# Kernel optimization log

Measured on AMD Instinct MI355X. Metric: run time of the kernel, lower is better.

## Reference

```python
import jax, jax.numpy as jnp
import numpy as np

EMBED_DIM = 1024
NUM_HEADS = 16
HEAD_DIM = EMBED_DIM // NUM_HEADS
B, L = 2, 2048
SCALE = HEAD_DIM ** -0.5


def setup_inputs() -> dict:
    key = jax.random.key(0)
    ks = jax.random.split(key, 8)
    x = jax.random.normal(ks[0], (B, L, EMBED_DIM), dtype=jnp.float32)
    phylo_dists = jax.random.uniform(ks[1], (B, L), dtype=jnp.float32)
    alibi_bias = jax.random.normal(ks[2], (NUM_HEADS, L, L), dtype=jnp.float32) * 0.02
    # causal mask: 1 where attending allowed (j <= i), broadcast over B,H
    attn_mask = (jnp.arange(L)[:, None] >= jnp.arange(L)[None, :])[None, None]
    # learned params (Linear stores weight as [out, in]; y = x @ W.T + b)
    qkv_w = jax.random.normal(ks[3], (3 * EMBED_DIM, EMBED_DIM), dtype=jnp.float32) * (EMBED_DIM ** -0.5)
    qkv_b = jnp.zeros((3 * EMBED_DIM,), dtype=jnp.float32)
    out_w = jax.random.normal(ks[4], (EMBED_DIM, EMBED_DIM), dtype=jnp.float32) * (EMBED_DIM ** -0.5)
    out_b = jnp.zeros((EMBED_DIM,), dtype=jnp.float32)
    phylo_alpha = jnp.float32(0.5)
    return {"x": x, "phylo_dists": phylo_dists, "alibi_bias": alibi_bias,
            "attn_mask": attn_mask, "qkv_w": qkv_w, "qkv_b": qkv_b,
            "out_w": out_w, "out_b": out_b, "phylo_alpha": phylo_alpha}


def reference(x, phylo_dists, alibi_bias, attn_mask, qkv_w, qkv_b, out_w, out_b, phylo_alpha):
    Bm, Lm, D = x.shape
    qkv = (x @ qkv_w.T + qkv_b).reshape(Bm, Lm, 3, NUM_HEADS, HEAD_DIM)
    qkv = jnp.transpose(qkv, (2, 0, 3, 1, 4))  # [3, B, H, L, hd]
    q, k, v = qkv[0], qkv[1], qkv[2]
    # phylo temperature: scalar per batch element
    phylo_scalar = phylo_dists.mean(axis=-1).reshape(Bm, 1, 1, 1)
    temp = jnp.clip(1.0 + phylo_alpha * phylo_scalar, 1e-6, None)
    scores = jnp.einsum('bhqd,bhkd->bhqk', q, k) * (SCALE * temp)
    scores = scores + alibi_bias[None]  # [B,H,L,L]
    scores = jnp.where(attn_mask, scores, -jnp.inf)
    attn = jax.nn.softmax(scores, axis=-1)
    out = jnp.einsum('bhqk,bhkd->bhqd', attn, v)
    out = jnp.transpose(out, (0, 2, 1, 3)).reshape(Bm, Lm, D)
    return out @ out_w.T + out_b
```

## Files before the change

kernel.cpp:

```cpp
#include <hip/hip_runtime.h>
#include <hip/hip_bf16.h>

typedef __attribute__((ext_vector_type(8))) short bf16x8;
typedef __attribute__((ext_vector_type(4))) float f32x4;
typedef __attribute__((ext_vector_type(4))) float f4v;
typedef __attribute__((ext_vector_type(4))) short s4v;

__device__ __forceinline__ short f2bf(float f) {
    union { __hip_bfloat16 h; short s; } u;
    u.h = __float2bfloat16(f);
    return u.s;
}

__device__ __forceinline__ void gload_lds16(const void* g, void* l) {
    __builtin_amdgcn_global_load_lds(
        (const __attribute__((address_space(1))) void*)g,
        (__attribute__((address_space(3))) void*)l,
        16, 0, 0);
}

#define MFMA16(a, b, c) __builtin_amdgcn_mfma_f32_16x16x32_bf16((a), (b), (c), 0, 0, 0)

__global__ void prep_kernel(const float* __restrict__ x,
                            const float* __restrict__ qw,
                            const float* __restrict__ ow,
                            const float* __restrict__ pd,
                            const float* __restrict__ alphap,
                            s4v* __restrict__ xb, s4v* __restrict__ qb,
                            s4v* __restrict__ ob, float* __restrict__ scales) {
    __shared__ float wsum[4];
    if (blockIdx.x >= 2048) {
        int b = blockIdx.x - 2048;
        float s = 0.f;
        for (int i = threadIdx.x; i < 2048; i += 256) s += pd[b * 2048 + i];
        for (int o = 32; o; o >>= 1) s += __shfl_down(s, o);
        if ((threadIdx.x & 63) == 0) wsum[threadIdx.x >> 6] = s;
        __syncthreads();
        if (threadIdx.x == 0) {
            float t = wsum[0] + wsum[1] + wsum[2] + wsum[3];
            float mean = t * (1.0f / 2048.0f);
            float temp = fmaxf(1.0f + alphap[0] * mean, 1e-6f);
            scales[b] = 0.125f * temp;
        }
        return;
    }
    #pragma unroll
    for (int j = 0; j < 4; ++j) {
        int idx = blockIdx.x * 1024 + j * 256 + threadIdx.x;
        const f4v* src;
        s4v* dst;
        int off;
        if (idx < 1048576)      { src = (const f4v*)x;  dst = xb; off = idx; }
        else if (idx < 1835008) { src = (const f4v*)qw; dst = qb; off = idx - 1048576; }
        else                    { src = (const f4v*)ow; dst = ob; off = idx - 1835008; }
        f4v v = src[off];
        s4v o;
        #pragma unroll
        for (int k = 0; k < 4; ++k) o[k] = f2bf(v[k]);
        dst[off] = o;
    }
}

template<int BF16_OUT, int NF>
__global__ __launch_bounds__(256, 2)
void gemm_nt(const __hip_bfloat16* __restrict__ A,
             const __hip_bfloat16* __restrict__ Bw,
             const float* __restrict__ bias,
             void* __restrict__ Cv,
             int M, int N, int K) {
    __shared__ short sA[128 * 64];
    __shared__ short sB[NF * 32 * 64];
    const int tid = threadIdx.x;
    const int wave = tid >> 6, lane = tid & 63;
    const int g = lane >> 4, c = lane & 15;
    const int wr = wave >> 1, wc = wave & 1;
    const long m0 = (long)blockIdx.y * 128, n0 = (long)blockIdx.x * (NF * 32);

    f32x4 acc[4][NF];
    #pragma unroll
    for (int m = 0; m < 4; ++m)
        #pragma unroll
        for (int n = 0; n < NF; ++n) acc[m][n] = f32x4{0.f, 0.f, 0.f, 0.f};

    for (int k0 = 0; k0 < K; k0 += 64) {
        #pragma unroll
        for (int i = 0; i < 4; ++i) {
            int cb = (i * 4 + wave) * 64;
            int chunk = cb + lane;
            int row = chunk >> 3;
            int sc = ((chunk & 7) * 16) ^ ((row & 7) << 4);
            const char* gA = (const char*)(A + (m0 + row) * (long)K + k0) + sc;
            gload_lds16(gA, (char*)sA + cb * 16);
        }
        #pragma unroll
        for (int i = 0; i < NF; ++i) {
            int cb = (i * 4 + wave) * 64;
            int chunk = cb + lane;
            int row = chunk >> 3;
            int sc = ((chunk & 7) * 16) ^ ((row & 7) << 4);
            const char* gB = (const char*)(Bw + (n0 + row) * (long)K + k0) + sc;
            gload_lds16(gB, (char*)sB + cb * 16);
        }
        __syncthreads();
        #pragma unroll
        for (int s = 0; s < 2; ++s) {
            bf16x8 af[4], bfr[NF];
            #pragma unroll
            for (int m = 0; m < 4; ++m) {
                int row = wr * 64 + m * 16 + c;
                int kb = (s * 64 + g * 16) ^ ((row & 7) << 4);
                af[m] = *(const bf16x8*)((const char*)sA + row * 128 + kb);
            }
            #pragma unroll
            for (int n = 0; n < NF; ++n) {
                int row = wc * (NF * 16) + n * 16 + c;
                int kb = (s * 64 + g * 16) ^ ((row & 7) << 4);
                bfr[n] = *(const bf16x8*)((const char*)sB + row * 128 + kb);
            }
            #pragma unroll
            for (int m = 0; m < 4; ++m)
                #pragma unroll
                for (int n = 0; n < NF; ++n)
                    acc[m][n] = MFMA16(af[m], bfr[n], acc[m][n]);
        }
        __syncthreads();
    }

    #pragma unroll
    for (int m = 0; m < 4; ++m) {
        #pragma unroll
        for (int n = 0; n < NF; ++n) {
            long col = n0 + wc * (NF * 16) + n * 16 + c;
            float bv = bias[col];
            #pragma unroll
            for (int r = 0; r < 4; ++r) {
                long row = m0 + wr * 64 + m * 16 + g * 4 + r;
                float v = acc[m][n][r] + bv;
                if (BF16_OUT)
                    ((__hip_bfloat16*)Cv)[row * N + col] = __float2bfloat16(v);
                else
                    ((float*)Cv)[row * N + col] = v;
            }
        }
    }
}


__device__ __forceinline__ void compute_tile(
    const short* sKc, const short* sVtc, short* sPw,
    bf16x8 qf0, bf16x8 qf1,
    f32x4 (&acc_o)[4], f32x4& accL, float (&m)[4],
    const float (&ab)[4][4],
    float scale, int qi0, int kv0, bool diag, int g, int c)
{
    f32x4 accs[4];
    const int swz = (c & 7) << 4;
    __builtin_amdgcn_s_setprio(1);
    #pragma unroll
    for (int nf = 0; nf < 4; ++nf) {
        const char* kb = (const char*)sKc + (nf * 16 + c) * 128;
        bf16x8 kf0 = *(const bf16x8*)(kb + ((g * 16) ^ swz));
        bf16x8 kf1 = *(const bf16x8*)(kb + ((64 + g * 16) ^ swz));
        accs[nf] = f32x4{0.f, 0.f, 0.f, 0.f};
        accs[nf] = MFMA16(qf0, kf0, accs[nf]);
        accs[nf] = MFMA16(qf1, kf1, accs[nf]);
    }
    __builtin_amdgcn_s_setprio(0);
    float s[4][4], pmax[4];
    bool ok = true;
    #pragma unroll
    for (int r = 0; r < 4; ++r) {
        int qi = qi0 + r;
        #pragma unroll
        for (int nf = 0; nf < 4; ++nf) {
            float sv = fmaf(accs[nf][r], scale, ab[nf][r]);
            if (diag && (kv0 + nf * 16 + c > qi)) sv = -1e30f;
            s[r][nf] = sv;
        }
        pmax[r] = fmaxf(fmaxf(s[r][0], s[r][1]), fmaxf(s[r][2], s[r][3]));
        ok = ok && (pmax[r] <= m[r] + 8.0f);
    }
    if (!__all(ok)) {
        #pragma unroll
        for (int r = 0; r < 4; ++r) {
            float mx = pmax[r];
            mx = fmaxf(mx, __shfl_xor(mx, 1));
            mx = fmaxf(mx, __shfl_xor(mx, 2));
            mx = fmaxf(mx, __shfl_xor(mx, 4));
            mx = fmaxf(mx, __shfl_xor(mx, 8));
            float mn = fmaxf(m[r], mx);
            float alpha = __expf(m[r] - mn);
            m[r] = mn;
            accL[r] *= alpha;
            #pragma unroll
            for (int d = 0; d < 4; ++d) acc_o[d][r] *= alpha;
        }
    }
    #pragma unroll
    for (int r = 0; r < 4; ++r)
        #pragma unroll
        for (int nf = 0; nf < 4; ++nf)
            sPw[(g * 4 + r) * 72 + nf * 16 + c] = f2bf(__expf(s[r][nf] - m[r]));
    asm volatile("s_waitcnt lgkmcnt(0)" ::: "memory");
    bf16x8 pf0 = *(const bf16x8*)((const char*)sPw + c * 144 + g * 16);
    bf16x8 pf1 = *(const bf16x8*)((const char*)sPw + c * 144 + 64 + g * 16);
    const short ONE = 0x3F80;
    const bf16x8 ones = {ONE, ONE, ONE, ONE, ONE, ONE, ONE, ONE};
    __builtin_amdgcn_s_setprio(1);
    accL = MFMA16(pf0, ones, accL);
    accL = MFMA16(pf1, ones, accL);
    #pragma unroll
    for (int d = 0; d < 4; ++d) {
        const char* vb = (const char*)sVtc + (d * 16 + c) * 144;
        bf16x8 vf0 = *(const bf16x8*)(vb + g * 16);
        bf16x8 vf1 = *(const bf16x8*)(vb + 64 + g * 16);
        acc_o[d] = MFMA16(pf0, vf0, acc_o[d]);
        acc_o[d] = MFMA16(pf1, vf1, acc_o[d]);
    }
    __builtin_amdgcn_s_setprio(0);
}

__global__ __launch_bounds__(256, 3)
void attn_kernel(const __hip_bfloat16* __restrict__ qkv,
                 const float* __restrict__ alibi,
                 const float* __restrict__ scales,
                 __hip_bfloat16* __restrict__ out) {
    __shared__ short sK[2][64 * 64];
    __shared__ short sVt[2][64 * 72];
    __shared__ short sP[4][16 * 72];

    const int h = blockIdx.x, b = blockIdx.y;
    const int qt = 31 - blockIdx.z;
    const int nIter = qt + 1;
    const int tid = threadIdx.x;
    const int wave = tid >> 6, lane = tid & 63;
    const int g = lane >> 4, c = lane & 15;
    const float scale = scales[b];
    const long base_bl = (long)b * 2048;

    const int q0 = qt * 64 + wave * 16;

    const __hip_bfloat16* qrow = qkv + (base_bl + q0 + c) * 3072 + h * 64;
    bf16x8 qf0 = *(const bf16x8*)(qrow + g * 8);
    bf16x8 qf1 = *(const bf16x8*)(qrow + 32 + g * 8);

    const __hip_bfloat16* kg = qkv + base_bl * 3072 + 1024 + h * 64;
    const __hip_bfloat16* vg = qkv + base_bl * 3072 + 2048 + h * 64;
    const float* ab_base = alibi + (long)h * 2048 * 2048 + (long)(q0 + g * 4) * 2048;

    const int p2 = tid & 31;
    const int d0 = (tid >> 5) * 8;
    const __hip_bfloat16* vrow = vg + (long)(2 * p2) * 3072 + d0;

    f32x4 acc[4], accL;
    float m[4];
    #pragma unroll
    for (int d = 0; d < 4; ++d) acc[d] = f32x4{0.f, 0.f, 0.f, 0.f};
    accL = f32x4{0.f, 0.f, 0.f, 0.f};
    #pragma unroll
    for (int r = 0; r < 4; ++r) m[r] = -3e38f;

    float ab[4][4], abn[4][4];

    {
        #pragma unroll
        for (int i = 0; i < 2; ++i) {
            int cb = (i * 4 + wave) * 64;
            int chunk = cb + lane;
            int row = chunk >> 3;
            int sc = ((chunk & 7) * 16) ^ ((row & 7) << 4);
            gload_lds16((const char*)(kg + (long)row * 3072) + sc,
                        (char*)sK[0] + cb * 16);
        }
        bf16x8 va = *(const bf16x8*)vrow;
        bf16x8 vb = *(const bf16x8*)(vrow + 3072);
        #pragma unroll
        for (int j = 0; j < 8; ++j) {
            unsigned pk = ((unsigned)(unsigned short)va[j]) |
                          (((unsigned)(unsigned short)vb[j]) << 16);
            *(unsigned*)((char*)sVt[0] + (d0 + j) * 144 + p2 * 4) = pk;
        }
        #pragma unroll
        for (int nf = 0; nf < 4; ++nf)
            #pragma unroll
            for (int r = 0; r < 4; ++r) {
                ab[nf][r] = ab_base[(long)r * 2048 + nf * 16 + c];
                abn[nf][r] = 0.f;
            }
    }
    __syncthreads();

    for (int t = 0; t < nIter; ++t) {
        const int cur = t & 1;
        const int kv0 = t * 64;
        bf16x8 va, vb;
        const bool haveNext = (t + 1 < nIter);
        if (haveNext) {
            #pragma unroll
            for (int i = 0; i < 2; ++i) {
                int cb = (i * 4 + wave) * 64;
                int chunk = cb + lane;
                int row = chunk >> 3;
                int sc = ((chunk & 7) * 16) ^ ((row & 7) << 4);
                gload_lds16((const char*)(kg + (long)(kv0 + 64 + row) * 3072) + sc,
                            (char*)sK[cur ^ 1] + cb * 16);
            }
            const __hip_bfloat16* vp = vrow + (long)(kv0 + 64) * 3072;
            va = *(const bf16x8*)vp;
            vb = *(const bf16x8*)(vp + 3072);
            #pragma unroll
            for (int nf = 0; nf < 4; ++nf)
                #pragma unroll
                for (int r = 0; r < 4; ++r)
                    abn[nf][r] = ab_base[(long)r * 2048 + kv0 + 64 + nf * 16 + c];
        }

        compute_tile(sK[cur], sVt[cur], &sP[wave][0], qf0, qf1,
                     acc, accL, m, ab, scale, q0 + g * 4, kv0, t == qt, g, c);

        if (haveNext) {
            #pragma unroll
            for (int j = 0; j < 8; ++j) {
                unsigned pk = ((unsigned)(unsigned short)va[j]) |
                              (((unsigned)(unsigned short)vb[j]) << 16);
                *(unsigned*)((char*)sVt[cur ^ 1] + (d0 + j) * 144 + p2 * 4) = pk;
            }
        }
        __syncthreads();
        #pragma unroll
        for (int nf = 0; nf < 4; ++nf)
            #pragma unroll
            for (int r = 0; r < 4; ++r)
                ab[nf][r] = abn[nf][r];
    }

    __hip_bfloat16* op = out + (base_bl + q0 + g * 4) * 1024 + h * 64;
    #pragma unroll
    for (int r = 0; r < 4; ++r) {
        float inv = 1.0f / accL[r];
        #pragma unroll
        for (int d = 0; d < 4; ++d)
            op[(long)r * 1024 + d * 16 + c] = __float2bfloat16(acc[d][r] * inv);
    }
}

extern "C" void kernel_launch(void* const* d_in, const int* in_sizes, int n_in,
                              void* d_out, int out_size, void* d_ws, size_t ws_size,
                              hipStream_t stream) {
    const float* x      = (const float*)d_in[0];
    const float* phylo  = (const float*)d_in[1];
    const float* alibi  = (const float*)d_in[2];
    const float* qkv_w  = (const float*)d_in[4];
    const float* qkv_b  = (const float*)d_in[5];
    const float* out_w  = (const float*)d_in[6];
    const float* out_b  = (const float*)d_in[7];
    const float* alphap = (const float*)d_in[8];

    char* ws = (char*)d_ws;
    __hip_bfloat16* xbf   = (__hip_bfloat16*)(ws);
    __hip_bfloat16* qwbf  = (__hip_bfloat16*)(ws + (8l << 20));
    __hip_bfloat16* owbf  = (__hip_bfloat16*)(ws + (14l << 20));
    __hip_bfloat16* qkvbf = (__hip_bfloat16*)(ws + (16l << 20));
    __hip_bfloat16* aobf  = (__hip_bfloat16*)(ws + (40l << 20));
    float* scales         = (float*)(ws + (48l << 20));

    prep_kernel<<<2050, 256, 0, stream>>>(x, qkv_w, out_w, phylo, alphap,
                                          (s4v*)xbf, (s4v*)qwbf, (s4v*)owbf, scales);

    gemm_nt<1, 4><<<dim3(24, 32), 256, 0, stream>>>(xbf, qwbf, qkv_b, qkvbf,
                                                    4096, 3072, 1024);
    attn_kernel<<<dim3(16, 2, 32), 256, 0, stream>>>(qkvbf, alibi, scales, aobf);
    gemm_nt<0, 2><<<dim3(16, 32), 256, 0, stream>>>(aobf, owbf, out_b, d_out,
                                                    4096, 1024, 1024);
}
```

Baseline: 127.8 us.

## Compute transposed scores so P stays in registers, dropping LDS round-trip

Swaps the MFMA operands so each lane holds one query's scores across key positions. The exponentiated probabilities can then be fed directly as the B operand of 16x16x16 MFMAs for the PV product, with no write and read through per-wave shared memory. Row sums are now taken with register adds and two shuffles instead of extra MFMAs against a ones vector, and the V stride is changed to 74. In exchange the PV product uses twice as many smaller-K MFMAs, and the alibi loads and output stores change access patterns.

Result: slower. 214.0 us (+67.4%).

```diff
diff --git a/kernel.cpp b/kernel.cpp
--- a/kernel.cpp
+++ b/kernel.cpp
@@ -2,6 +2,7 @@
 #include <hip/hip_bf16.h>
 
 typedef __attribute__((ext_vector_type(8))) short bf16x8;
+typedef __attribute__((ext_vector_type(4))) short bf16x4;
 typedef __attribute__((ext_vector_type(4))) float f32x4;
 typedef __attribute__((ext_vector_type(4))) float f4v;
 typedef __attribute__((ext_vector_type(4))) short s4v;
@@ -20,6 +21,7 @@
 }
 
 #define MFMA16(a, b, c) __builtin_amdgcn_mfma_f32_16x16x32_bf16((a), (b), (c), 0, 0, 0)
+#define MFMA16K16(a, b, c) __builtin_amdgcn_mfma_f32_16x16x16bf16_1k((a), (b), (c), 0, 0, 0)
 
 __global__ void prep_kernel(const float* __restrict__ x,
                             const float* __restrict__ qw,
@@ -146,79 +148,7 @@
 }
 
 
-__device__ __forceinline__ void compute_tile(
-    const short* sKc, const short* sVtc, short* sPw,
-    bf16x8 qf0, bf16x8 qf1,
-    f32x4 (&acc_o)[4], f32x4& accL, float (&m)[4],
-    const float (&ab)[4][4],
-    float scale, int qi0, int kv0, bool diag, int g, int c)
-{
-    f32x4 accs[4];
-    const int swz = (c & 7) << 4;
-    __builtin_amdgcn_s_setprio(1);
-    #pragma unroll
-    for (int nf = 0; nf < 4; ++nf) {
-        const char* kb = (const char*)sKc + (nf * 16 + c) * 128;
-        bf16x8 kf0 = *(const bf16x8*)(kb + ((g * 16) ^ swz));
-        bf16x8 kf1 = *(const bf16x8*)(kb + ((64 + g * 16) ^ swz));
-        accs[nf] = f32x4{0.f, 0.f, 0.f, 0.f};
-        accs[nf] = MFMA16(qf0, kf0, accs[nf]);
-        accs[nf] = MFMA16(qf1, kf1, accs[nf]);
-    }
-    __builtin_amdgcn_s_setprio(0);
-    float s[4][4], pmax[4];
-    bool ok = true;
-    #pragma unroll
-    for (int r = 0; r < 4; ++r) {
-        int qi = qi0 + r;
-        #pragma unroll
-        for (int nf = 0; nf < 4; ++nf) {
-            float sv = fmaf(accs[nf][r], scale, ab[nf][r]);
-            if (diag && (kv0 + nf * 16 + c > qi)) sv = -1e30f;
-            s[r][nf] = sv;
-        }
-        pmax[r] = fmaxf(fmaxf(s[r][0], s[r][1]), fmaxf(s[r][2], s[r][3]));
-        ok = ok && (pmax[r] <= m[r] + 8.0f);
-    }
-    if (!__all(ok)) {
-        #pragma unroll
-        for (int r = 0; r < 4; ++r) {
-            float mx = pmax[r];
-            mx = fmaxf(mx, __shfl_xor(mx, 1));
-            mx = fmaxf(mx, __shfl_xor(mx, 2));
-            mx = fmaxf(mx, __shfl_xor(mx, 4));
-            mx = fmaxf(mx, __shfl_xor(mx, 8));
-            float mn = fmaxf(m[r], mx);
-            float alpha = __expf(m[r] - mn);
-            m[r] = mn;
-            accL[r] *= alpha;
-            #pragma unroll
-            for (int d = 0; d < 4; ++d) acc_o[d][r] *= alpha;
-        }
-    }
-    #pragma unroll
-    for (int r = 0; r < 4; ++r)
-        #pragma unroll
-        for (int nf = 0; nf < 4; ++nf)
-            sPw[(g * 4 + r) * 72 + nf * 16 + c] = f2bf(__expf(s[r][nf] - m[r]));
-    asm volatile("s_waitcnt lgkmcnt(0)" ::: "memory");
-    bf16x8 pf0 = *(const bf16x8*)((const char*)sPw + c * 144 + g * 16);
-    bf16x8 pf1 = *(const bf16x8*)((const char*)sPw + c * 144 + 64 + g * 16);
-    const short ONE = 0x3F80;
-    const bf16x8 ones = {ONE, ONE, ONE, ONE, ONE, ONE, ONE, ONE};
-    __builtin_amdgcn_s_setprio(1);
-    accL = MFMA16(pf0, ones, accL);
-    accL = MFMA16(pf1, ones, accL);
-    #pragma unroll
-    for (int d = 0; d < 4; ++d) {
-        const char* vb = (const char*)sVtc + (d * 16 + c) * 144;
-        bf16x8 vf0 = *(const bf16x8*)(vb + g * 16);
-        bf16x8 vf1 = *(const bf16x8*)(vb + 64 + g * 16);
-        acc_o[d] = MFMA16(pf0, vf0, acc_o[d]);
-        acc_o[d] = MFMA16(pf1, vf1, acc_o[d]);
-    }
-    __builtin_amdgcn_s_setprio(0);
-}
+#define VSTRIDE 74
 
 __global__ __launch_bounds__(256, 3)
 void attn_kernel(const __hip_bfloat16* __restrict__ qkv,
@@ -226,8 +156,7 @@
                  const float* __restrict__ scales,
                  __hip_bfloat16* __restrict__ out) {
     __shared__ short sK[2][64 * 64];
-    __shared__ short sVt[2][64 * 72];
-    __shared__ short sP[4][16 * 72];
+    __shared__ short sVt[2][64 * VSTRIDE];
 
     const int h = blockIdx.x, b = blockIdx.y;
     const int qt = 31 - blockIdx.z;
@@ -238,27 +167,25 @@
     const float scale = scales[b];
     const long base_bl = (long)b * 2048;
 
-    const int q0 = qt * 64 + wave * 16;
-
-    const __hip_bfloat16* qrow = qkv + (base_bl + q0 + c) * 3072 + h * 64;
+    const int q0w = qt * 64 + wave * 16;
+    const int q_lane = q0w + c;
+
+    const __hip_bfloat16* qrow = qkv + (base_bl + q_lane) * 3072 + h * 64;
     bf16x8 qf0 = *(const bf16x8*)(qrow + g * 8);
     bf16x8 qf1 = *(const bf16x8*)(qrow + 32 + g * 8);
 
     const __hip_bfloat16* kg = qkv + base_bl * 3072 + 1024 + h * 64;
     const __hip_bfloat16* vg = qkv + base_bl * 3072 + 2048 + h * 64;
-    const float* ab_base = alibi + (long)h * 2048 * 2048 + (long)(q0 + g * 4) * 2048;
+    const float* ab_base = alibi + (long)h * 2048 * 2048 + (long)q_lane * 2048 + g * 4;
 
     const int p2 = tid & 31;
     const int d0 = (tid >> 5) * 8;
     const __hip_bfloat16* vrow = vg + (long)(2 * p2) * 3072 + d0;
 
-    f32x4 acc[4], accL;
-    float m[4];
+    f32x4 acc[4];
+    float accL = 0.f, m = -3e38f;
     #pragma unroll
     for (int d = 0; d < 4; ++d) acc[d] = f32x4{0.f, 0.f, 0.f, 0.f};
-    accL = f32x4{0.f, 0.f, 0.f, 0.f};
-    #pragma unroll
-    for (int r = 0; r < 4; ++r) m[r] = -3e38f;
 
     float ab[4][4], abn[4][4];
 
@@ -278,13 +205,13 @@
         for (int j = 0; j < 8; ++j) {
             unsigned pk = ((unsigned)(unsigned short)va[j]) |
                           (((unsigned)(unsigned short)vb[j]) << 16);
-            *(unsigned*)((char*)sVt[0] + (d0 + j) * 144 + p2 * 4) = pk;
+            *(unsigned*)((char*)sVt[0] + (d0 + j) * (VSTRIDE * 2) + p2 * 4) = pk;
         }
         #pragma unroll
         for (int nf = 0; nf < 4; ++nf)
             #pragma unroll
             for (int r = 0; r < 4; ++r) {
-                ab[nf][r] = ab_base[(long)r * 2048 + nf * 16 + c];
+                ab[nf][r] = ab_base[nf * 16 + r];
                 abn[nf][r] = 0.f;
             }
     }
@@ -312,18 +239,91 @@
             for (int nf = 0; nf < 4; ++nf)
                 #pragma unroll
                 for (int r = 0; r < 4; ++r)
-                    abn[nf][r] = ab_base[(long)r * 2048 + kv0 + 64 + nf * 16 + c];
-        }
-
-        compute_tile(sK[cur], sVt[cur], &sP[wave][0], qf0, qf1,
-                     acc, accL, m, ab, scale, q0 + g * 4, kv0, t == qt, g, c);
+                    abn[nf][r] = ab_base[kv0 + 64 + nf * 16 + r];
+        }
+
+        {
+            const short* sKc = sK[cur];
+            const short* sVtc = sVt[cur];
+            const bool diag = (t == qt);
+            f32x4 accs[4];
+            const int swz = (c & 7) << 4;
+            __builtin_amdgcn_s_setprio(1);
+            #pragma unroll
+            for (int nf = 0; nf < 4; ++nf) {
+                const char* kb = (const char*)sKc + (nf * 16 + c) * 128;
+                bf16x8 kf0 = *(const bf16x8*)(kb + ((g * 16) ^ swz));
+                bf16x8 kf1 = *(const bf16x8*)(kb + ((64 + g * 16) ^ swz));
+                accs[nf] = f32x4{0.f, 0.f, 0.f, 0.f};
+                accs[nf] = MFMA16(kf0, qf0, accs[nf]);
+                accs[nf] = MFMA16(kf1, qf1, accs[nf]);
+            }
+            __builtin_amdgcn_s_setprio(0);
+
+            float s[4][4];
+            float pmax = -3e38f;
+            #pragma unroll
+            for (int nf = 0; nf < 4; ++nf)
+                #pragma unroll
+                for (int r = 0; r < 4; ++r) {
+                    float sv = fmaf(accs[nf][r], scale, ab[nf][r]);
+                    if (diag && (kv0 + nf * 16 + g * 4 + r > q_lane)) sv = -1e30f;
+                    s[nf][r] = sv;
+                    pmax = fmaxf(pmax, sv);
+                }
+            bool ok = (pmax <= m + 8.0f);
+            if (!__all(ok)) {
+                float mx = fmaxf(pmax, __shfl_xor(pmax, 16));
+                mx = fmaxf(mx, __shfl_xor(mx, 32));
+                float mn = fmaxf(m, mx);
+                float alpha = __expf(m - mn);
+                m = mn;
+                accL *= alpha;
+                #pragma unroll
+                for (int d = 0; d < 4; ++d)
+                    #pragma unroll
+                    for (int r = 0; r < 4; ++r) acc[d][r] *= alpha;
+            }
+            unsigned pw[4][2];
+            float ls = 0.f;
+            #pragma unroll
+            for (int nf = 0; nf < 4; ++nf) {
+                float e0 = __expf(s[nf][0] - m);
+                float e1 = __expf(s[nf][1] - m);
+                float e2 = __expf(s[nf][2] - m);
+                float e3 = __expf(s[nf][3] - m);
+                ls += (e0 + e1) + (e2 + e3);
+                pw[nf][0] = ((unsigned)(unsigned short)f2bf(e0)) |
+                            (((unsigned)(unsigned short)f2bf(e1)) << 16);
+                pw[nf][1] = ((unsigned)(unsigned short)f2bf(e2)) |
+                            (((unsigned)(unsigned short)f2bf(e3)) << 16);
+            }
+            ls += __shfl_xor(ls, 16);
+            ls += __shfl_xor(ls, 32);
+            accL += ls;
+
+            __builtin_amdgcn_s_setprio(1);
+            #pragma unroll
+            for (int df = 0; df < 4; ++df) {
+                const char* vb2 = (const char*)sVtc + (df * 16 + c) * (VSTRIDE * 2);
+                #pragma unroll
+                for (int nf = 0; nf < 4; ++nf) {
+                    bf16x4 vf = *(const bf16x4*)(vb2 + (nf * 16 + g * 4) * 2);
+                    union { unsigned w[2]; bf16x4 v; } pu;
+                    pu.w[0] = pw[nf][0];
+                    pu.w[1] = pw[nf][1];
+                    acc[df] = MFMA16K16(vf, pu.v, acc[df]);
+                }
+            }
+            __builtin_amdgcn_s_setprio(0);
+        }
 
         if (haveNext) {
             #pragma unroll
             for (int j = 0; j < 8; ++j) {
                 unsigned pk = ((unsigned)(unsigned short)va[j]) |
                               (((unsigned)(unsigned short)vb[j]) << 16);
-                *(unsigned*)((char*)sVt[cur ^ 1] + (d0 + j) * 144 + p2 * 4) = pk;
+                *(unsigned*)((char*)sVt[cur ^ 1] + (d0 + j) * (VSTRIDE * 2) + p2 * 4) = pk;
             }
         }
         __syncthreads();
@@ -334,13 +334,14 @@
                 ab[nf][r] = abn[nf][r];
     }
 
-    __hip_bfloat16* op = out + (base_bl + q0 + g * 4) * 1024 + h * 64;
-    #pragma unroll
-    for (int r = 0; r < 4; ++r) {
-        float inv = 1.0f / accL[r];
-        #pragma unroll
-        for (int d = 0; d < 4; ++d)
-            op[(long)r * 1024 + d * 16 + c] = __float2bfloat16(acc[d][r] * inv);
+    __hip_bfloat16* op = out + (base_bl + q_lane) * 1024 + h * 64;
+    float inv = 1.0f / accL;
+    #pragma unroll
+    for (int df = 0; df < 4; ++df) {
+        s4v o;
+        #pragma unroll
+        for (int r = 0; r < 4; ++r) o[r] = f2bf(acc[df][r] * inv);
+        *(s4v*)(op + df * 16 + g * 4) = o;
     }
 }
 
```

## Split KV range for long causal query tiles and merge partials

Applied to the files above, without the earlier changes.

The upper 16 query tiles of the causal attention now run as two blocks, each covering half of the KV range, instead of one long block. Partial outputs and their (max, sum) statistics go to workspace, and a new merge kernel combines them with log-sum-exp weights. The aim is to shorten the longest blocks and balance work across CUs. The cost is an extra kernel launch, extra global traffic for the partials, and bf16 rounding of the partials before the merge.

Measured after the change: 136.8 us. 1.07x slower.

```diff
diff --git a/kernel.cpp b/kernel.cpp
--- a/kernel.cpp
+++ b/kernel.cpp
@@ -10,6 +10,12 @@
     union { __hip_bfloat16 h; short s; } u;
     u.h = __float2bfloat16(f);
     return u.s;
+}
+
+__device__ __forceinline__ float bf2f(short s) {
+    union { short s; __hip_bfloat16 h; } u;
+    u.s = s;
+    return __bfloat162float(u.h);
 }
 
 __device__ __forceinline__ void gload_lds16(const void* g, void* l) {
@@ -224,14 +230,29 @@
 void attn_kernel(const __hip_bfloat16* __restrict__ qkv,
                  const float* __restrict__ alibi,
                  const float* __restrict__ scales,
-                 __hip_bfloat16* __restrict__ out) {
+                 __hip_bfloat16* __restrict__ out,
+                 __hip_bfloat16* __restrict__ pO,
+                 float2* __restrict__ pML) {
     __shared__ short sK[2][64 * 64];
     __shared__ short sVt[2][64 * 72];
     __shared__ short sP[4][16 * 72];
 
     const int h = blockIdx.x, b = blockIdx.y;
-    const int qt = 31 - blockIdx.z;
-    const int nIter = qt + 1;
+    const int z = blockIdx.z;
+    int qt, t0, t1, split;
+    if (z < 32) {
+        qt = 31 - (z >> 1);
+        split = z & 1;
+        int nIter = qt + 1;
+        int half = nIter >> 1;
+        t0 = split ? half : 0;
+        t1 = split ? nIter : half;
+    } else {
+        qt = 47 - z;
+        split = -1;
+        t0 = 0;
+        t1 = qt + 1;
+    }
     const int tid = threadIdx.x;
     const int wave = tid >> 6, lane = tid & 63;
     const int g = lane >> 4, c = lane & 15;
@@ -263,38 +284,40 @@
     float ab[4][4], abn[4][4];
 
     {
+        const int kvp = t0 * 64;
         #pragma unroll
         for (int i = 0; i < 2; ++i) {
             int cb = (i * 4 + wave) * 64;
             int chunk = cb + lane;
             int row = chunk >> 3;
             int sc = ((chunk & 7) * 16) ^ ((row & 7) << 4);
-            gload_lds16((const char*)(kg + (long)row * 3072) + sc,
-                        (char*)sK[0] + cb * 16);
-        }
-        bf16x8 va = *(const bf16x8*)vrow;
-        bf16x8 vb = *(const bf16x8*)(vrow + 3072);
+            gload_lds16((const char*)(kg + (long)(kvp + row) * 3072) + sc,
+                        (char*)sK[t0 & 1] + cb * 16);
+        }
+        const __hip_bfloat16* vp = vrow + (long)kvp * 3072;
+        bf16x8 va = *(const bf16x8*)vp;
+        bf16x8 vb = *(const bf16x8*)(vp + 3072);
         #pragma unroll
         for (int j = 0; j < 8; ++j) {
             unsigned pk = ((unsigned)(unsigned short)va[j]) |
                           (((unsigned)(unsigned short)vb[j]) << 16);
-            *(unsigned*)((char*)sVt[0] + (d0 + j) * 144 + p2 * 4) = pk;
+            *(unsigned*)((char*)sVt[t0 & 1] + (d0 + j) * 144 + p2 * 4) = pk;
         }
         #pragma unroll
         for (int nf = 0; nf < 4; ++nf)
             #pragma unroll
             for (int r = 0; r < 4; ++r) {
-                ab[nf][r] = ab_base[(long)r * 2048 + nf * 16 + c];
+                ab[nf][r] = ab_base[(long)r * 2048 + kvp + nf * 16 + c];
                 abn[nf][r] = 0.f;
             }
     }
     __syncthreads();
 
-    for (int t = 0; t < nIter; ++t) {
+    for (int t = t0; t < t1; ++t) {
         const int cur = t & 1;
         const int kv0 = t * 64;
         bf16x8 va, vb;
-        const bool haveNext = (t + 1 < nIter);
+        const bool haveNext = (t + 1 < t1);
         if (haveNext) {
             #pragma unroll
             for (int i = 0; i < 2; ++i) {
@@ -334,13 +357,58 @@
                 ab[nf][r] = abn[nf][r];
     }
 
-    __hip_bfloat16* op = out + (base_bl + q0 + g * 4) * 1024 + h * 64;
-    #pragma unroll
-    for (int r = 0; r < 4; ++r) {
-        float inv = 1.0f / accL[r];
-        #pragma unroll
-        for (int d = 0; d < 4; ++d)
-            op[(long)r * 1024 + d * 16 + c] = __float2bfloat16(acc[d][r] * inv);
+    if (split >= 0) {
+        const long pbase = ((((long)b * 16 + h) * 16 + (qt - 16)) * 2 + split) * 64;
+        #pragma unroll
+        for (int r = 0; r < 4; ++r) {
+            int ql = wave * 16 + g * 4 + r;
+            float invL = 1.0f / accL[r];
+            __hip_bfloat16* pp = pO + (pbase + ql) * 64;
+            #pragma unroll
+            for (int d = 0; d < 4; ++d)
+                pp[d * 16 + c] = __float2bfloat16(acc[d][r] * invL);
+            if (c == 0) pML[pbase + ql] = float2{m[r], accL[r]};
+        }
+    } else {
+        __hip_bfloat16* op = out + (base_bl + q0 + g * 4) * 1024 + h * 64;
+        #pragma unroll
+        for (int r = 0; r < 4; ++r) {
+            float inv = 1.0f / accL[r];
+            #pragma unroll
+            for (int d = 0; d < 4; ++d)
+                op[(long)r * 1024 + d * 16 + c] = __float2bfloat16(acc[d][r] * inv);
+        }
+    }
+}
+
+__global__ void merge_kernel(const __hip_bfloat16* __restrict__ pO,
+                             const float2* __restrict__ pML,
+                             __hip_bfloat16* __restrict__ out) {
+    const int qt = 16 + blockIdx.x;
+    const int h = blockIdx.y, b = blockIdx.z;
+    const int t = threadIdx.x;
+    const int row = t >> 2;
+    const int c0 = (t & 3) << 4;
+    const long base = (((long)b * 16 + h) * 16 + blockIdx.x) * 2;
+    float2 ml1 = pML[(base + 0) * 64 + row];
+    float2 ml2 = pML[(base + 1) * 64 + row];
+    float M = fmaxf(ml1.x, ml2.x);
+    float w1 = __expf(ml1.x - M) * ml1.y;
+    float w2 = __expf(ml2.x - M) * ml2.y;
+    float inv = 1.0f / (w1 + w2);
+    w1 *= inv;
+    w2 *= inv;
+    const bf16x8* p1 = (const bf16x8*)(pO + ((base + 0) * 64 + row) * 64 + c0);
+    const bf16x8* p2 = (const bf16x8*)(pO + ((base + 1) * 64 + row) * 64 + c0);
+    __hip_bfloat16* op = out + ((long)b * 2048 + (long)qt * 64 + row) * 1024 + h * 64 + c0;
+    #pragma unroll
+    for (int k = 0; k < 2; ++k) {
+        bf16x8 a = p1[k], bv = p2[k];
+        bf16x8 o;
+        #pragma unroll
+        for (int j = 0; j < 8; ++j)
+            o[j] = f2bf(bf2f(a[j]) * w1 + bf2f(bv[j]) * w2);
+        *(bf16x8*)(op + k * 8) = o;
     }
 }
 
@@ -363,13 +431,17 @@
     __hip_bfloat16* qkvbf = (__hip_bfloat16*)(ws + (16l << 20));
     __hip_bfloat16* aobf  = (__hip_bfloat16*)(ws + (40l << 20));
     float* scales         = (float*)(ws + (48l << 20));
+    __hip_bfloat16* pO    = (__hip_bfloat16*)(ws);
+    float2* pML           = (float2*)(ws + (8l << 20));
 
     prep_kernel<<<2050, 256, 0, stream>>>(x, qkv_w, out_w, phylo, alphap,
                                           (s4v*)xbf, (s4v*)qwbf, (s4v*)owbf, scales);
 
     gemm_nt<1, 4><<<dim3(24, 32), 256, 0, stream>>>(xbf, qwbf, qkv_b, qkvbf,
                                                     4096, 3072, 1024);
-    attn_kernel<<<dim3(16, 2, 32), 256, 0, stream>>>(qkvbf, alibi, scales, aobf);
+    attn_kernel<<<dim3(16, 2, 48), 256, 0, stream>>>(qkvbf, alibi, scales, aobf,
+                                                     pO, pML);
+    merge_kernel<<<dim3(16, 16, 2), 256, 0, stream>>>(pO, pML, aobf);
     gemm_nt<0, 2><<<dim3(16, 32), 256, 0, stream>>>(aobf, owbf, out_b, d_out,
                                                     4096, 1024, 1024);
 }
```

## Pair complementary causal query tiles in one 512-thread attention block

Applied to the files above, without the earlier changes.

Each attention block now has 8 waves and handles two query tiles, p and 31-p, so every block walks the same number of KV tiles and the causal work is balanced across blocks. The K/V tiles staged in LDS are shared by both query tiles, which halves K/V global loads per query. Waves on the shorter tile skip compute once past their diagonal but still hit the barriers. The grid halves to 512 blocks, which lowers parallelism and raises register and LDS pressure per block.

Result: no change. 129.8 us (+1.5%).

```diff
diff --git a/kernel.cpp b/kernel.cpp
--- a/kernel.cpp
+++ b/kernel.cpp
@@ -220,25 +220,26 @@
     __builtin_amdgcn_s_setprio(0);
 }
 
-__global__ __launch_bounds__(256, 3)
+__global__ __launch_bounds__(512, 4)
 void attn_kernel(const __hip_bfloat16* __restrict__ qkv,
                  const float* __restrict__ alibi,
                  const float* __restrict__ scales,
                  __hip_bfloat16* __restrict__ out) {
     __shared__ short sK[2][64 * 64];
     __shared__ short sVt[2][64 * 72];
-    __shared__ short sP[4][16 * 72];
+    __shared__ short sP[8][16 * 72];
 
     const int h = blockIdx.x, b = blockIdx.y;
-    const int qt = 31 - blockIdx.z;
-    const int nIter = qt + 1;
+    const int p = blockIdx.z;
     const int tid = threadIdx.x;
     const int wave = tid >> 6, lane = tid & 63;
     const int g = lane >> 4, c = lane & 15;
+    const int tileQt = (wave < 4) ? p : (31 - p);
+    const int nIter = 32 - p;
     const float scale = scales[b];
     const long base_bl = (long)b * 2048;
 
-    const int q0 = qt * 64 + wave * 16;
+    const int q0 = tileQt * 64 + (wave & 3) * 16;
 
     const __hip_bfloat16* qrow = qkv + (base_bl + q0 + c) * 3072 + h * 64;
     bf16x8 qf0 = *(const bf16x8*)(qrow + g * 8);
@@ -249,8 +250,9 @@
     const float* ab_base = alibi + (long)h * 2048 * 2048 + (long)(q0 + g * 4) * 2048;
 
     const int p2 = tid & 31;
-    const int d0 = (tid >> 5) * 8;
+    const int d0 = ((tid >> 5) & 7) * 8;
     const __hip_bfloat16* vrow = vg + (long)(2 * p2) * 3072 + d0;
+    const bool vstager = (tid < 256);
 
     f32x4 acc[4], accL;
     float m[4];
@@ -263,22 +265,20 @@
     float ab[4][4], abn[4][4];
 
     {
-        #pragma unroll
-        for (int i = 0; i < 2; ++i) {
-            int cb = (i * 4 + wave) * 64;
-            int chunk = cb + lane;
-            int row = chunk >> 3;
-            int sc = ((chunk & 7) * 16) ^ ((row & 7) << 4);
-            gload_lds16((const char*)(kg + (long)row * 3072) + sc,
-                        (char*)sK[0] + cb * 16);
-        }
-        bf16x8 va = *(const bf16x8*)vrow;
-        bf16x8 vb = *(const bf16x8*)(vrow + 3072);
-        #pragma unroll
-        for (int j = 0; j < 8; ++j) {
-            unsigned pk = ((unsigned)(unsigned short)va[j]) |
-                          (((unsigned)(unsigned short)vb[j]) << 16);
-            *(unsigned*)((char*)sVt[0] + (d0 + j) * 144 + p2 * 4) = pk;
+        int chunk = tid;
+        int row = chunk >> 3;
+        int sc = ((chunk & 7) * 16) ^ ((row & 7) << 4);
+        gload_lds16((const char*)(kg + (long)row * 3072) + sc,
+                    (char*)sK[0] + chunk * 16);
+        if (vstager) {
+            bf16x8 va = *(const bf16x8*)vrow;
+            bf16x8 vb = *(const bf16x8*)(vrow + 3072);
+            #pragma unroll
+            for (int j = 0; j < 8; ++j) {
+                unsigned pk = ((unsigned)(unsigned short)va[j]) |
+                              (((unsigned)(unsigned short)vb[j]) << 16);
+                *(unsigned*)((char*)sVt[0] + (d0 + j) * 144 + p2 * 4) = pk;
+            }
         }
         #pragma unroll
         for (int nf = 0; nf < 4; ++nf)
@@ -296,18 +296,18 @@
         bf16x8 va, vb;
         const bool haveNext = (t + 1 < nIter);
         if (haveNext) {
-            #pragma unroll
-            for (int i = 0; i < 2; ++i) {
-                int cb = (i * 4 + wave) * 64;
-                int chunk = cb + lane;
-                int row = chunk >> 3;
-                int sc = ((chunk & 7) * 16) ^ ((row & 7) << 4);
-                gload_lds16((const char*)(kg + (long)(kv0 + 64 + row) * 3072) + sc,
-                            (char*)sK[cur ^ 1] + cb * 16);
-            }
-            const __hip_bfloat16* vp = vrow + (long)(kv0 + 64) * 3072;
-            va = *(const bf16x8*)vp;
-            vb = *(const bf16x8*)(vp + 3072);
+            int chunk = tid;
+            int row = chunk >> 3;
+            int sc = ((chunk & 7) * 16) ^ ((row & 7) << 4);
+            gload_lds16((const char*)(kg + (long)(kv0 + 64 + row) * 3072) + sc,
+                        (char*)sK[cur ^ 1] + chunk * 16);
+            if (vstager) {
+                const __hip_bfloat16* vp = vrow + (long)(kv0 + 64) * 3072;
+                va = *(const bf16x8*)vp;
+                vb = *(const bf16x8*)(vp + 3072);
+            }
+        }
+        if (t + 1 <= tileQt) {
             #pragma unroll
             for (int nf = 0; nf < 4; ++nf)
                 #pragma unroll
@@ -315,10 +315,12 @@
                     abn[nf][r] = ab_base[(long)r * 2048 + kv0 + 64 + nf * 16 + c];
         }
 
-        compute_tile(sK[cur], sVt[cur], &sP[wave][0], qf0, qf1,
-                     acc, accL, m, ab, scale, q0 + g * 4, kv0, t == qt, g, c);
-
-        if (haveNext) {
+        if (t <= tileQt)
+            compute_tile(sK[cur], sVt[cur], &sP[wave][0], qf0, qf1,
+                         acc, accL, m, ab, scale, q0 + g * 4, kv0,
+                         t == tileQt, g, c);
+
+        if (haveNext && vstager) {
             #pragma unroll
             for (int j = 0; j < 8; ++j) {
                 unsigned pk = ((unsigned)(unsigned short)va[j]) |
@@ -369,7 +371,7 @@
 
     gemm_nt<1, 4><<<dim3(24, 32), 256, 0, stream>>>(xbf, qwbf, qkv_b, qkvbf,
                                                     4096, 3072, 1024);
-    attn_kernel<<<dim3(16, 2, 32), 256, 0, stream>>>(qkvbf, alibi, scales, aobf);
+    attn_kernel<<<dim3(16, 2, 16), 512, 0, stream>>>(qkvbf, alibi, scales, aobf);
     gemm_nt<0, 2><<<dim3(16, 32), 256, 0, stream>>>(aobf, owbf, out_b, d_out,
                                                     4096, 1024, 1024);
 }
```
